# Performance work log

Measured on AMD Instinct MI355X. Metric: run time of the kernel, lower is better.

## Reference

```python
import jax, jax.numpy as jnp
import numpy as np

B_, T_, DIM, HID, OUT, TAG = 128, 256, 512, 1024, 512, 64

def hard_sigmoid(x):
    return jnp.clip(0.2 * x + 0.5, 0.0, 1.0)

def setup_inputs() -> dict:
    key = jax.random.key(0)
    ks = jax.random.split(key, 8)
    s = 0.02  # weight scale for numerical stability under softmax
    return {
        "x": jax.random.normal(ks[0], (B_, T_, DIM), jnp.float32),
        "x0": jnp.zeros((B_, OUT), jnp.float32),
        "s0": jnp.zeros((B_, HID), jnp.float32),
        "W": jax.random.normal(ks[1], (OUT, 3 * HID), jnp.float32) * s,
        "U": jax.random.normal(ks[2], (HID, 3 * HID), jnp.float32) * s,
        "b": jnp.zeros((3 * HID,), jnp.float32),
        "W_x": jax.random.normal(ks[3], (HID, OUT), jnp.float32) * s,
        "b_x": jnp.zeros((OUT,), jnp.float32),
        "V_r": jax.random.normal(ks[4], (DIM, HID), jnp.float32) * s,
        "V_z": jax.random.normal(ks[5], (DIM, HID), jnp.float32) * s,
        "V_s": jax.random.normal(ks[6], (DIM, HID), jnp.float32) * s,
        "W_y": jax.random.normal(ks[7], (OUT, TAG), jnp.float32) * s,
        "b_y": jnp.zeros((TAG,), jnp.float32),
    }

def reference(x, x0, s0, W, U, b, W_x, b_x, V_r, V_z, V_s, W_y, b_y):
    h = HID
    W_r, W_z, W_s = W[:, :h], W[:, h:2*h], W[:, 2*h:]
    U_r, U_z, U_s = U[:, :h], U[:, h:2*h], U[:, 2*h:]
    b_r, b_z, b_s = b[:h], b[h:2*h], b[2*h:]

    def step(carry, inp):
        x_tm1, s_tm1 = carry
        xr = x_tm1 @ W_r + b_r + inp @ V_r
        xz = x_tm1 @ W_z + b_z + inp @ V_z
        r = hard_sigmoid(xr + s_tm1 @ U_r)
        z = hard_sigmoid(xz + s_tm1 @ U_z)
        xs = x_tm1 @ W_s + b_s + inp @ V_s
        s1 = jnp.tanh(xs + (r * s_tm1) @ U_s)
        s_t = (1.0 - z) * s_tm1 + z * s1
        x_t = jax.nn.softmax(s_t @ W_x + b_x, axis=-1)
        t_t = jax.nn.softmax(x_t @ W_y + b_y, axis=-1)
        return (x_t, s_t), t_t

    xs_seq = jnp.swapaxes(x, 0, 1)  # [T, B, dim]
    (_, _), t_seq = jax.lax.scan(step, (x0, s0), xs_seq)
    return jnp.swapaxes(t_seq, 0, 1)  # [B, T, tag]
```

## Files before the change

kernel.cpp:

```cpp
#include <hip/hip_runtime.h>
#include <math.h>

#define B_    128
#define T_    256
#define DIM_  512
#define HID_  1024
#define OUT_  512
#define TAG_  64
#define K3_   3072

typedef float f32x4 __attribute__((ext_vector_type(4)));
typedef short bf16x8 __attribute__((ext_vector_type(8)));

#define MFMA(a,b,c) __builtin_amdgcn_mfma_f32_16x16x32_bf16(a,b,c,0,0,0)

__device__ __forceinline__ unsigned short f2b(float f){
    unsigned int u = __float_as_uint(f);
    u = (u + 0x7fffu + ((u >> 16) & 1u)) >> 16;
    return (unsigned short)u;
}
__device__ __forceinline__ float hardsig(float x){
    return fminf(fmaxf(0.2f*x + 0.5f, 0.f), 1.f);
}
__device__ __forceinline__ bf16x8 ld8(const unsigned short* p){
    return *(const bf16x8*)p;
}
__device__ __forceinline__ bf16x8 ld8f(const float* p){
    float4 a = *(const float4*)p;
    float4 b = *(const float4*)(p + 4);
    bf16x8 r;
    r[0]=(short)f2b(a.x); r[1]=(short)f2b(a.y); r[2]=(short)f2b(a.z); r[3]=(short)f2b(a.w);
    r[4]=(short)f2b(b.x); r[5]=(short)f2b(b.y); r[6]=(short)f2b(b.z); r[7]=(short)f2b(b.w);
    return r;
}

__global__ __launch_bounds__(256) void k_tr(
    unsigned short* __restrict__ dst, const float* __restrict__ src,
    int K, int ld, int col_off)
{
    __shared__ float tile[32][33];
    const int kb = blockIdx.x * 32, nb = blockIdx.y * 32;
    const int tx = threadIdx.x & 31, ty = threadIdx.x >> 5;
    #pragma unroll
    for (int i = 0; i < 4; ++i){
        int kl = ty + i*8;
        tile[kl][tx] = src[(size_t)(kb + kl)*ld + col_off + nb + tx];
    }
    __syncthreads();
    #pragma unroll
    for (int i = 0; i < 4; ++i){
        int nl = ty + i*8;
        dst[(size_t)(nb + nl)*K + kb + tx] = f2b(tile[tx][nl]);
    }
}

__global__ __launch_bounds__(256) void k_cvtx(
    const float4* __restrict__ src, ushort4* __restrict__ dst, int n4)
{
    int i = blockIdx.x * 256 + threadIdx.x;
    if (i < n4){
        float4 v = src[i];
        ushort4 o;
        o.x = f2b(v.x); o.y = f2b(v.y); o.z = f2b(v.z); o.w = f2b(v.w);
        dst[i] = o;
    }
}

__global__ __launch_bounds__(256) void k_init(
    const float* __restrict__ x0, const float* __restrict__ s0,
    unsigned short* __restrict__ xbuf_b, float* __restrict__ sb0,
    unsigned short* __restrict__ s_b)
{
    int i = blockIdx.x * 256 + threadIdx.x;
    if (i < B_*OUT_) xbuf_b[i] = f2b(x0[i]);
    if (i < B_*HID_){ sb0[i] = s0[i]; s_b[i] = f2b(s0[i]); }
}

__global__ __launch_bounds__(256) void k_gemmA(
    const unsigned short* __restrict__ xbuf_b,
    const unsigned short* __restrict__ xb16,
    const float* __restrict__ xf,
    const unsigned short* __restrict__ s_b,
    const float* __restrict__ sp,
    const unsigned short* __restrict__ Wt,
    const unsigned short* __restrict__ Vrt,
    const unsigned short* __restrict__ Vzt,
    const unsigned short* __restrict__ Vst,
    const unsigned short* __restrict__ Urzt,
    const float* __restrict__ bias,
    float* __restrict__ pre,
    unsigned short* __restrict__ rs_b,
    int t, int use_xb)
{
    const int wid  = (blockIdx.x * 256 + threadIdx.x) >> 6;
    const int lane = threadIdx.x & 63;
    const int mt   = wid & 7;
    const int nt   = wid >> 3;
    const int n0   = nt * 32;
    const int nseg = n0 >> 10;
    const int l15  = lane & 15;
    const int kch  = lane >> 4;
    const int arow = mt*16 + l15;
    f32x4 acc0 = {0.f,0.f,0.f,0.f};
    f32x4 acc1 = {0.f,0.f,0.f,0.f};

    {
        const unsigned short* ab = xbuf_b + arow*OUT_ + kch*8;
        const unsigned short* b0 = Wt + (size_t)(n0 + l15)*OUT_ + kch*8;
        const unsigned short* b1 = b0 + 16*OUT_;
        #pragma unroll 4
        for (int kb = 0; kb < OUT_; kb += 32){
            bf16x8 a = ld8(ab + kb);
            acc0 = MFMA(a, ld8(b0 + kb), acc0);
            acc1 = MFMA(a, ld8(b1 + kb), acc1);
        }
    }
    {
        const unsigned short* Vt = (nseg==0) ? Vrt : ((nseg==1) ? Vzt : Vst);
        const int nl = n0 - (nseg << 10);
        const unsigned short* b0 = Vt + (size_t)(nl + l15)*DIM_ + kch*8;
        const unsigned short* b1 = b0 + 16*DIM_;
        if (use_xb){
            const unsigned short* ab = xb16 + ((size_t)arow*T_ + t)*DIM_ + kch*8;
            #pragma unroll 4
            for (int kb = 0; kb < DIM_; kb += 32){
                bf16x8 a = ld8(ab + kb);
                acc0 = MFMA(a, ld8(b0 + kb), acc0);
                acc1 = MFMA(a, ld8(b1 + kb), acc1);
            }
        } else {
            const float* af = xf + ((size_t)arow*T_ + t)*DIM_ + kch*8;
            #pragma unroll 2
            for (int kb = 0; kb < DIM_; kb += 32){
                bf16x8 a = ld8f(af + kb);
                acc0 = MFMA(a, ld8(b0 + kb), acc0);
                acc1 = MFMA(a, ld8(b1 + kb), acc1);
            }
        }
    }
    if (nseg < 2){
        const unsigned short* ab = s_b + arow*HID_ + kch*8;
        const unsigned short* b0 = Urzt + (size_t)(n0 + l15)*HID_ + kch*8;
        const unsigned short* b1 = b0 + 16*HID_;
        #pragma unroll 4
        for (int kb = 0; kb < HID_; kb += 32){
            bf16x8 a = ld8(ab + kb);
            acc0 = MFMA(a, ld8(b0 + kb), acc0);
            acc1 = MFMA(a, ld8(b1 + kb), acc1);
        }
    }
    const int rbase = mt*16 + kch*4;
    #pragma unroll
    for (int half = 0; half < 2; ++half){
        f32x4 acc = half ? acc1 : acc0;
        const int col = n0 + half*16 + l15;
        const float bv = bias[col];
        #pragma unroll
        for (int q = 0; q < 4; ++q){
            const int r = rbase + q;
            const float v = acc[q] + bv;
            if (nseg == 0){
                float rs = hardsig(v) * sp[r*HID_ + col];
                rs_b[r*HID_ + col] = f2b(rs);
            } else {
                pre[(size_t)r*K3_ + col] = v;
            }
        }
    }
}

__global__ __launch_bounds__(256) void k_gemmB(
    const unsigned short* __restrict__ rs_b,
    const unsigned short* __restrict__ Ust,
    const float* __restrict__ pre,
    const float* __restrict__ sp,
    float* __restrict__ snf,
    unsigned short* __restrict__ s_b)
{
    const int wid  = (blockIdx.x * 256 + threadIdx.x) >> 6;
    const int lane = threadIdx.x & 63;
    const int mt = wid & 7;
    const int nt = wid >> 3;
    const int n0 = nt * 32;
    const int l15 = lane & 15;
    const int kch = lane >> 4;
    const int arow = mt*16 + l15;
    f32x4 acc0 = {0.f,0.f,0.f,0.f};
    f32x4 acc1 = {0.f,0.f,0.f,0.f};
    const unsigned short* ab = rs_b + arow*HID_ + kch*8;
    const unsigned short* b0 = Ust + (size_t)(n0 + l15)*HID_ + kch*8;
    const unsigned short* b1 = b0 + 16*HID_;
    #pragma unroll 4
    for (int kb = 0; kb < HID_; kb += 32){
        bf16x8 a = ld8(ab + kb);
        acc0 = MFMA(a, ld8(b0 + kb), acc0);
        acc1 = MFMA(a, ld8(b1 + kb), acc1);
    }
    const int rbase = mt*16 + kch*4;
    #pragma unroll
    for (int half = 0; half < 2; ++half){
        f32x4 acc = half ? acc1 : acc0;
        const int col = n0 + half*16 + l15;
        #pragma unroll
        for (int q = 0; q < 4; ++q){
            const int r = rbase + q;
            float z  = hardsig(pre[(size_t)r*K3_ + HID_ + col]);
            float xs = pre[(size_t)r*K3_ + 2*HID_ + col];
            float so = sp[r*HID_ + col];
            float s1 = tanhf(xs + acc[q]);
            float sn = (1.f - z)*so + z*s1;
            snf[r*HID_ + col] = sn;
            s_b[r*HID_ + col] = f2b(sn);
        }
    }
}

__global__ __launch_bounds__(256) void k_gemmC(
    const unsigned short* __restrict__ s_b,
    const unsigned short* __restrict__ Wxt,
    const float* __restrict__ bx,
    float* __restrict__ logits)
{
    const int wid  = (blockIdx.x * 256 + threadIdx.x) >> 6;
    const int lane = threadIdx.x & 63;
    const int mt = wid & 7;
    const int nt = wid >> 3;
    const int n0 = nt * 32;
    const int l15 = lane & 15;
    const int kch = lane >> 4;
    const int arow = mt*16 + l15;
    f32x4 acc0 = {0.f,0.f,0.f,0.f};
    f32x4 acc1 = {0.f,0.f,0.f,0.f};
    const unsigned short* ab = s_b + arow*HID_ + kch*8;
    const unsigned short* b0 = Wxt + (size_t)(n0 + l15)*HID_ + kch*8;
    const unsigned short* b1 = b0 + 16*HID_;
    #pragma unroll 4
    for (int kb = 0; kb < HID_; kb += 32){
        bf16x8 a = ld8(ab + kb);
        acc0 = MFMA(a, ld8(b0 + kb), acc0);
        acc1 = MFMA(a, ld8(b1 + kb), acc1);
    }
    const int rbase = mt*16 + kch*4;
    #pragma unroll
    for (int half = 0; half < 2; ++half){
        f32x4 acc = half ? acc1 : acc0;
        const int col = n0 + half*16 + l15;
        #pragma unroll
        for (int q = 0; q < 4; ++q){
            logits[(rbase + q)*OUT_ + col] = acc[q] + bx[col];
        }
    }
}

__global__ __launch_bounds__(256) void k_soft(
    const float* __restrict__ logits, const float* __restrict__ Wy,
    const float* __restrict__ by, unsigned short* __restrict__ xbuf_b,
    float* __restrict__ out, int t)
{
    __shared__ float xs[512];
    __shared__ float red[256];
    const int r = blockIdx.x, tid = threadIdx.x;
    float v0 = logits[r*OUT_ + tid];
    float v1 = logits[r*OUT_ + 256 + tid];
    red[tid] = fmaxf(v0, v1);
    __syncthreads();
    for (int s = 128; s > 0; s >>= 1){
        if (tid < s) red[tid] = fmaxf(red[tid], red[tid+s]);
        __syncthreads();
    }
    float mx = red[0];
    __syncthreads();
    float e0 = expf(v0 - mx), e1 = expf(v1 - mx);
    red[tid] = e0 + e1;
    __syncthreads();
    for (int s = 128; s > 0; s >>= 1){
        if (tid < s) red[tid] += red[tid+s];
        __syncthreads();
    }
    float inv = 1.f / red[0];
    __syncthreads();
    float x0v = e0*inv, x1v = e1*inv;
    xs[tid]       = x0v;
    xs[tid + 256] = x1v;
    xbuf_b[r*OUT_ + tid]       = f2b(x0v);
    xbuf_b[r*OUT_ + 256 + tid] = f2b(x1v);
    __syncthreads();
    const int j = tid & 63, part = tid >> 6;
    float p = 0.f;
    const int k0 = part * 128;
    #pragma unroll 4
    for (int k = k0; k < k0 + 128; ++k) p += xs[k] * Wy[k*TAG_ + j];
    red[tid] = p;
    __syncthreads();
    if (tid < 64){
        float tl = red[tid] + red[tid+64] + red[tid+128] + red[tid+192] + by[tid];
        float wm = tl;
        #pragma unroll
        for (int off = 32; off > 0; off >>= 1) wm = fmaxf(wm, __shfl_xor(wm, off));
        float ex = expf(tl - wm);
        float sm = ex;
        #pragma unroll
        for (int off = 32; off > 0; off >>= 1) sm += __shfl_xor(sm, off);
        out[((long)r*T_ + t)*TAG_ + tid] = ex / sm;
    }
}

extern "C" void kernel_launch(void* const* d_in, const int* in_sizes, int n_in,
                              void* d_out, int out_size, void* d_ws, size_t ws_size,
                              hipStream_t stream){
    const float* x   = (const float*)d_in[0];
    const float* x0  = (const float*)d_in[1];
    const float* s0  = (const float*)d_in[2];
    const float* W   = (const float*)d_in[3];
    const float* U   = (const float*)d_in[4];
    const float* b   = (const float*)d_in[5];
    const float* Wx  = (const float*)d_in[6];
    const float* bx  = (const float*)d_in[7];
    const float* Vr  = (const float*)d_in[8];
    const float* Vz  = (const float*)d_in[9];
    const float* Vs  = (const float*)d_in[10];
    const float* Wy  = (const float*)d_in[11];
    const float* by  = (const float*)d_in[12];
    float* out = (float*)d_out;

    char* ws = (char*)d_ws;
    size_t off = 0;
    auto alloc = [&](size_t bytes) -> size_t {
        size_t o = off; off = (off + bytes + 255) & ~(size_t)255; return o;
    };
    unsigned short* Wt     = (unsigned short*)(ws + alloc((size_t)K3_*OUT_*2));
    unsigned short* Urzt   = (unsigned short*)(ws + alloc((size_t)2048*HID_*2));
    unsigned short* Ust    = (unsigned short*)(ws + alloc((size_t)HID_*HID_*2));
    unsigned short* Vrt    = (unsigned short*)(ws + alloc((size_t)HID_*DIM_*2));
    unsigned short* Vzt    = (unsigned short*)(ws + alloc((size_t)HID_*DIM_*2));
    unsigned short* Vst    = (unsigned short*)(ws + alloc((size_t)HID_*DIM_*2));
    unsigned short* Wxt    = (unsigned short*)(ws + alloc((size_t)OUT_*HID_*2));
    unsigned short* xbuf_b = (unsigned short*)(ws + alloc((size_t)B_*OUT_*2));
    unsigned short* s_b    = (unsigned short*)(ws + alloc((size_t)B_*HID_*2));
    unsigned short* rs_b   = (unsigned short*)(ws + alloc((size_t)B_*HID_*2));
    float* sb0    = (float*)(ws + alloc((size_t)B_*HID_*4));
    float* sb1    = (float*)(ws + alloc((size_t)B_*HID_*4));
    float* pre    = (float*)(ws + alloc((size_t)B_*K3_*4));
    float* logits = (float*)(ws + alloc((size_t)B_*OUT_*4));
    size_t base_need = off;
    unsigned short* xb16 = (unsigned short*)(ws + alloc((size_t)B_*T_*DIM_*2));
    const int use_xb = (off <= ws_size) ? 1 : 0;
    (void)base_need;

    k_tr<<<dim3(OUT_/32, K3_/32),  256, 0, stream>>>(Wt,   W,  OUT_, K3_, 0);
    k_tr<<<dim3(HID_/32, 2048/32), 256, 0, stream>>>(Urzt, U,  HID_, K3_, 0);
    k_tr<<<dim3(HID_/32, HID_/32), 256, 0, stream>>>(Ust,  U,  HID_, K3_, 2048);
    k_tr<<<dim3(DIM_/32, HID_/32), 256, 0, stream>>>(Vrt,  Vr, DIM_, HID_, 0);
    k_tr<<<dim3(DIM_/32, HID_/32), 256, 0, stream>>>(Vzt,  Vz, DIM_, HID_, 0);
    k_tr<<<dim3(DIM_/32, HID_/32), 256, 0, stream>>>(Vst,  Vs, DIM_, HID_, 0);
    k_tr<<<dim3(HID_/32, OUT_/32), 256, 0, stream>>>(Wxt,  Wx, HID_, OUT_, 0);
    if (use_xb){
        int n4 = B_*T_*DIM_/4;
        k_cvtx<<<(n4 + 255)/256, 256, 0, stream>>>((const float4*)x, (ushort4*)xb16, n4);
    }
    k_init<<<(B_*HID_ + 255)/256, 256, 0, stream>>>(x0, s0, xbuf_b, sb0, s_b);

    for (int t = 0; t < T_; ++t){
        float* sp = (t & 1) ? sb1 : sb0;
        float* sn = (t & 1) ? sb0 : sb1;
        k_gemmA<<<192, 256, 0, stream>>>(xbuf_b, xb16, x, s_b, sp,
                                         Wt, Vrt, Vzt, Vst, Urzt, b,
                                         pre, rs_b, t, use_xb);
        k_gemmB<<<64, 256, 0, stream>>>(rs_b, Ust, pre, sp, sn, s_b);
        k_gemmC<<<32, 256, 0, stream>>>(s_b, Wxt, bx, logits);
        k_soft <<<128, 256, 0, stream>>>(logits, Wy, by, xbuf_b, out, t);
    }
}
```

Before: 17.24 ms.

## Replace per-timestep kernel launches with one persistent cooperative kernel

Replaces the 1024 small per-step launches (four kernels for each of 256 steps) with a single persistent cooperative kernel of 96 workgroups. The stages are separated by an atomic-counter grid barrier with acquire/release semantics. This removes launch overhead and the inter-kernel gaps on the serial recurrence. In exchange it adds a spin-barrier cost four times per step, and later stages leave many workgroups idle. A launch failure falls back to the old multi-kernel loop.

```diff
diff --git a/kernel.cpp b/kernel.cpp
--- a/kernel.cpp
+++ b/kernel.cpp
@@ -8,6 +8,7 @@
 #define OUT_  512
 #define TAG_  64
 #define K3_   3072
+#define NWG_  96
 
 typedef float f32x4 __attribute__((ext_vector_type(4)));
 typedef short bf16x8 __attribute__((ext_vector_type(8)));
@@ -34,6 +35,16 @@
     return r;
 }
 
+__device__ __forceinline__ void gsync(unsigned* cnt, unsigned target){
+    __syncthreads();
+    if (threadIdx.x == 0){
+        __hip_atomic_fetch_add(cnt, 1u, __ATOMIC_RELEASE, __HIP_MEMORY_SCOPE_AGENT);
+        while (__hip_atomic_load(cnt, __ATOMIC_ACQUIRE, __HIP_MEMORY_SCOPE_AGENT) < target)
+            __builtin_amdgcn_s_sleep(2);
+    }
+    __syncthreads();
+}
+
 __global__ __launch_bounds__(256) void k_tr(
     unsigned short* __restrict__ dst, const float* __restrict__ src,
     int K, int ld, int col_off)
@@ -76,34 +87,234 @@
     if (i < B_*HID_){ sb0[i] = s0[i]; s_b[i] = f2b(s0[i]); }
 }
 
+__global__ __launch_bounds__(512, 1) void k_persist(
+    const unsigned short* __restrict__ xb16, const float* __restrict__ xf, int use_xb,
+    const unsigned short* __restrict__ Wt,  const unsigned short* __restrict__ Vrt,
+    const unsigned short* __restrict__ Vzt, const unsigned short* __restrict__ Vst,
+    const unsigned short* __restrict__ Urzt,const unsigned short* __restrict__ Ust,
+    const unsigned short* __restrict__ Wxt,
+    const float* __restrict__ bias, const float* __restrict__ bx,
+    const float* __restrict__ Wy,   const float* __restrict__ by,
+    unsigned short* __restrict__ xbuf_b, unsigned short* __restrict__ s_b,
+    unsigned short* __restrict__ rs_b,
+    float* __restrict__ sb0, float* __restrict__ sb1,
+    float* __restrict__ pre, float* __restrict__ logits,
+    float* __restrict__ out, unsigned* __restrict__ cnt)
+{
+    const int wg   = blockIdx.x;
+    const int tid  = threadIdx.x;
+    const int lane = tid & 63;
+    const int wv   = tid >> 6;
+    const int l15  = lane & 15;
+    const int kch  = lane >> 4;
+    unsigned target = 0;
+
+    __shared__ float sm_xs[512];
+    __shared__ float sm_red[512];
+
+    for (int t = 0; t < T_; ++t){
+        const float* sp = (t & 1) ? sb1 : sb0;
+        float*       sn = (t & 1) ? sb0 : sb1;
+
+        {
+            const int n0   = wg * 32;
+            const int nseg = n0 >> 10;
+            const int arow = wv*16 + l15;
+            f32x4 acc0 = {0.f,0.f,0.f,0.f};
+            f32x4 acc1 = {0.f,0.f,0.f,0.f};
+            {
+                const unsigned short* ab = xbuf_b + arow*OUT_ + kch*8;
+                const unsigned short* b0 = Wt + (size_t)(n0 + l15)*OUT_ + kch*8;
+                const unsigned short* b1 = b0 + 16*OUT_;
+                #pragma unroll 4
+                for (int kb = 0; kb < OUT_; kb += 32){
+                    bf16x8 a = ld8(ab + kb);
+                    acc0 = MFMA(a, ld8(b0 + kb), acc0);
+                    acc1 = MFMA(a, ld8(b1 + kb), acc1);
+                }
+            }
+            {
+                const unsigned short* Vt = (nseg==0) ? Vrt : ((nseg==1) ? Vzt : Vst);
+                const int nl = n0 - (nseg << 10);
+                const unsigned short* b0 = Vt + (size_t)(nl + l15)*DIM_ + kch*8;
+                const unsigned short* b1 = b0 + 16*DIM_;
+                if (use_xb){
+                    const unsigned short* ab = xb16 + ((size_t)arow*T_ + t)*DIM_ + kch*8;
+                    #pragma unroll 4
+                    for (int kb = 0; kb < DIM_; kb += 32){
+                        bf16x8 a = ld8(ab + kb);
+                        acc0 = MFMA(a, ld8(b0 + kb), acc0);
+                        acc1 = MFMA(a, ld8(b1 + kb), acc1);
+                    }
+                } else {
+                    const float* af = xf + ((size_t)arow*T_ + t)*DIM_ + kch*8;
+                    #pragma unroll 2
+                    for (int kb = 0; kb < DIM_; kb += 32){
+                        bf16x8 a = ld8f(af + kb);
+                        acc0 = MFMA(a, ld8(b0 + kb), acc0);
+                        acc1 = MFMA(a, ld8(b1 + kb), acc1);
+                    }
+                }
+            }
+            if (nseg < 2){
+                const unsigned short* ab = s_b + arow*HID_ + kch*8;
+                const unsigned short* b0 = Urzt + (size_t)(n0 + l15)*HID_ + kch*8;
+                const unsigned short* b1 = b0 + 16*HID_;
+                #pragma unroll 4
+                for (int kb = 0; kb < HID_; kb += 32){
+                    bf16x8 a = ld8(ab + kb);
+                    acc0 = MFMA(a, ld8(b0 + kb), acc0);
+                    acc1 = MFMA(a, ld8(b1 + kb), acc1);
+                }
+            }
+            const int rbase = wv*16 + kch*4;
+            #pragma unroll
+            for (int half = 0; half < 2; ++half){
+                f32x4 acc = half ? acc1 : acc0;
+                const int col = n0 + half*16 + l15;
+                const float bv = bias[col];
+                #pragma unroll
+                for (int q = 0; q < 4; ++q){
+                    const int r = rbase + q;
+                    const float v = acc[q] + bv;
+                    if (nseg == 0){
+                        float rs = hardsig(v) * sp[r*HID_ + col];
+                        rs_b[r*HID_ + col] = f2b(rs);
+                    } else {
+                        pre[(size_t)r*K3_ + col] = v;
+                    }
+                }
+            }
+        }
+        target += NWG_; gsync(cnt, target);
+
+        if (wg < 32){
+            const int n0 = wg * 32;
+            const int arow = wv*16 + l15;
+            f32x4 acc0 = {0.f,0.f,0.f,0.f};
+            f32x4 acc1 = {0.f,0.f,0.f,0.f};
+            const unsigned short* ab = rs_b + arow*HID_ + kch*8;
+            const unsigned short* b0 = Ust + (size_t)(n0 + l15)*HID_ + kch*8;
+            const unsigned short* b1 = b0 + 16*HID_;
+            #pragma unroll 4
+            for (int kb = 0; kb < HID_; kb += 32){
+                bf16x8 a = ld8(ab + kb);
+                acc0 = MFMA(a, ld8(b0 + kb), acc0);
+                acc1 = MFMA(a, ld8(b1 + kb), acc1);
+            }
+            const int rbase = wv*16 + kch*4;
+            #pragma unroll
+            for (int half = 0; half < 2; ++half){
+                f32x4 acc = half ? acc1 : acc0;
+                const int col = n0 + half*16 + l15;
+                #pragma unroll
+                for (int q = 0; q < 4; ++q){
+                    const int r = rbase + q;
+                    float z  = hardsig(pre[(size_t)r*K3_ + HID_ + col]);
+                    float xs = pre[(size_t)r*K3_ + 2*HID_ + col];
+                    float so = sp[r*HID_ + col];
+                    float s1 = tanhf(xs + acc[q]);
+                    float snv = (1.f - z)*so + z*s1;
+                    sn[r*HID_ + col] = snv;
+                    s_b[r*HID_ + col] = f2b(snv);
+                }
+            }
+        }
+        target += NWG_; gsync(cnt, target);
+
+        if (wg < 16){
+            const int n0 = wg * 32;
+            const int arow = wv*16 + l15;
+            f32x4 acc0 = {0.f,0.f,0.f,0.f};
+            f32x4 acc1 = {0.f,0.f,0.f,0.f};
+            const unsigned short* ab = s_b + arow*HID_ + kch*8;
+            const unsigned short* b0 = Wxt + (size_t)(n0 + l15)*HID_ + kch*8;
+            const unsigned short* b1 = b0 + 16*HID_;
+            #pragma unroll 4
+            for (int kb = 0; kb < HID_; kb += 32){
+                bf16x8 a = ld8(ab + kb);
+                acc0 = MFMA(a, ld8(b0 + kb), acc0);
+                acc1 = MFMA(a, ld8(b1 + kb), acc1);
+            }
+            const int rbase = wv*16 + kch*4;
+            #pragma unroll
+            for (int half = 0; half < 2; ++half){
+                f32x4 acc = half ? acc1 : acc0;
+                const int col = n0 + half*16 + l15;
+                #pragma unroll
+                for (int q = 0; q < 4; ++q){
+                    logits[(rbase + q)*OUT_ + col] = acc[q] + bx[col];
+                }
+            }
+        }
+        target += NWG_; gsync(cnt, target);
+
+        for (int r = wg; r < B_; r += NWG_){
+            float v = logits[r*OUT_ + tid];
+            float m = v;
+            #pragma unroll
+            for (int off = 32; off > 0; off >>= 1) m = fmaxf(m, __shfl_xor(m, off));
+            if (lane == 0) sm_red[wv] = m;
+            __syncthreads();
+            float mx = sm_red[0];
+            #pragma unroll
+            for (int q = 1; q < 8; ++q) mx = fmaxf(mx, sm_red[q]);
+            float e = expf(v - mx);
+            float ssum = e;
+            #pragma unroll
+            for (int off = 32; off > 0; off >>= 1) ssum += __shfl_xor(ssum, off);
+            __syncthreads();
+            if (lane == 0) sm_red[wv] = ssum;
+            __syncthreads();
+            float tot = 0.f;
+            #pragma unroll
+            for (int q = 0; q < 8; ++q) tot += sm_red[q];
+            float xv = e / tot;
+            sm_xs[tid] = xv;
+            xbuf_b[r*OUT_ + tid] = f2b(xv);
+            __syncthreads();
+            const int tag = tid & 63, part = tid >> 6;
+            float p = 0.f;
+            const int k0 = part * 64;
+            #pragma unroll 4
+            for (int k = k0; k < k0 + 64; ++k) p += sm_xs[k] * Wy[k*TAG_ + tag];
+            sm_red[tid] = p;
+            __syncthreads();
+            if (tid < 64){
+                float tl = by[tid];
+                #pragma unroll
+                for (int q = 0; q < 8; ++q) tl += sm_red[q*64 + tid];
+                float wm = tl;
+                #pragma unroll
+                for (int off = 32; off > 0; off >>= 1) wm = fmaxf(wm, __shfl_xor(wm, off));
+                float ex = expf(tl - wm);
+                float sm = ex;
+                #pragma unroll
+                for (int off = 32; off > 0; off >>= 1) sm += __shfl_xor(sm, off);
+                out[((long)r*T_ + t)*TAG_ + tid] = ex / sm;
+            }
+            __syncthreads();
+        }
+        target += NWG_; gsync(cnt, target);
+    }
+}
+
 __global__ __launch_bounds__(256) void k_gemmA(
-    const unsigned short* __restrict__ xbuf_b,
-    const unsigned short* __restrict__ xb16,
-    const float* __restrict__ xf,
-    const unsigned short* __restrict__ s_b,
-    const float* __restrict__ sp,
-    const unsigned short* __restrict__ Wt,
-    const unsigned short* __restrict__ Vrt,
-    const unsigned short* __restrict__ Vzt,
-    const unsigned short* __restrict__ Vst,
-    const unsigned short* __restrict__ Urzt,
-    const float* __restrict__ bias,
-    float* __restrict__ pre,
-    unsigned short* __restrict__ rs_b,
-    int t, int use_xb)
+    const unsigned short* __restrict__ xbuf_b, const unsigned short* __restrict__ xb16,
+    const float* __restrict__ xf, const unsigned short* __restrict__ s_b,
+    const float* __restrict__ sp, const unsigned short* __restrict__ Wt,
+    const unsigned short* __restrict__ Vrt, const unsigned short* __restrict__ Vzt,
+    const unsigned short* __restrict__ Vst, const unsigned short* __restrict__ Urzt,
+    const float* __restrict__ bias, float* __restrict__ pre,
+    unsigned short* __restrict__ rs_b, int t, int use_xb)
 {
     const int wid  = (blockIdx.x * 256 + threadIdx.x) >> 6;
     const int lane = threadIdx.x & 63;
-    const int mt   = wid & 7;
-    const int nt   = wid >> 3;
-    const int n0   = nt * 32;
-    const int nseg = n0 >> 10;
-    const int l15  = lane & 15;
-    const int kch  = lane >> 4;
+    const int mt = wid & 7, nt = wid >> 3;
+    const int n0 = nt * 32, nseg = n0 >> 10;
+    const int l15 = lane & 15, kch = lane >> 4;
     const int arow = mt*16 + l15;
-    f32x4 acc0 = {0.f,0.f,0.f,0.f};
-    f32x4 acc1 = {0.f,0.f,0.f,0.f};
-
+    f32x4 acc0 = {0.f,0.f,0.f,0.f}, acc1 = {0.f,0.f,0.f,0.f};
     {
         const unsigned short* ab = xbuf_b + arow*OUT_ + kch*8;
         const unsigned short* b0 = Wt + (size_t)(n0 + l15)*OUT_ + kch*8;
@@ -170,23 +381,17 @@
 }
 
 __global__ __launch_bounds__(256) void k_gemmB(
-    const unsigned short* __restrict__ rs_b,
-    const unsigned short* __restrict__ Ust,
-    const float* __restrict__ pre,
-    const float* __restrict__ sp,
-    float* __restrict__ snf,
-    unsigned short* __restrict__ s_b)
+    const unsigned short* __restrict__ rs_b, const unsigned short* __restrict__ Ust,
+    const float* __restrict__ pre, const float* __restrict__ sp,
+    float* __restrict__ snf, unsigned short* __restrict__ s_b)
 {
     const int wid  = (blockIdx.x * 256 + threadIdx.x) >> 6;
     const int lane = threadIdx.x & 63;
-    const int mt = wid & 7;
-    const int nt = wid >> 3;
+    const int mt = wid & 7, nt = wid >> 3;
     const int n0 = nt * 32;
-    const int l15 = lane & 15;
-    const int kch = lane >> 4;
+    const int l15 = lane & 15, kch = lane >> 4;
     const int arow = mt*16 + l15;
-    f32x4 acc0 = {0.f,0.f,0.f,0.f};
-    f32x4 acc1 = {0.f,0.f,0.f,0.f};
+    f32x4 acc0 = {0.f,0.f,0.f,0.f}, acc1 = {0.f,0.f,0.f,0.f};
     const unsigned short* ab = rs_b + arow*HID_ + kch*8;
     const unsigned short* b0 = Ust + (size_t)(n0 + l15)*HID_ + kch*8;
     const unsigned short* b1 = b0 + 16*HID_;
@@ -208,29 +413,24 @@
             float xs = pre[(size_t)r*K3_ + 2*HID_ + col];
             float so = sp[r*HID_ + col];
             float s1 = tanhf(xs + acc[q]);
-            float sn = (1.f - z)*so + z*s1;
-            snf[r*HID_ + col] = sn;
-            s_b[r*HID_ + col] = f2b(sn);
+            float snv = (1.f - z)*so + z*s1;
+            snf[r*HID_ + col] = snv;
+            s_b[r*HID_ + col] = f2b(snv);
         }
     }
 }
 
 __global__ __launch_bounds__(256) void k_gemmC(
-    const unsigned short* __restrict__ s_b,
-    const unsigned short* __restrict__ Wxt,
-    const float* __restrict__ bx,
-    float* __restrict__ logits)
+    const unsigned short* __restrict__ s_b, const unsigned short* __restrict__ Wxt,
+    const float* __restrict__ bx, float* __restrict__ logits)
 {
     const int wid  = (blockIdx.x * 256 + threadIdx.x) >> 6;
     const int lane = threadIdx.x & 63;
-    const int mt = wid & 7;
-    const int nt = wid >> 3;
+    const int mt = wid & 7, nt = wid >> 3;
     const int n0 = nt * 32;
-    const int l15 = lane & 15;
-    const int kch = lane >> 4;
+    const int l15 = lane & 15, kch = lane >> 4;
     const int arow = mt*16 + l15;
-    f32x4 acc0 = {0.f,0.f,0.f,0.f};
-    f32x4 acc1 = {0.f,0.f,0.f,0.f};
+    f32x4 acc0 = {0.f,0.f,0.f,0.f}, acc1 = {0.f,0.f,0.f,0.f};
     const unsigned short* ab = s_b + arow*HID_ + kch*8;
     const unsigned short* b0 = Wxt + (size_t)(n0 + l15)*HID_ + kch*8;
     const unsigned short* b1 = b0 + 16*HID_;
@@ -280,9 +480,8 @@
     float inv = 1.f / red[0];
     __syncthreads();
     float x0v = e0*inv, x1v = e1*inv;
-    xs[tid]       = x0v;
-    xs[tid + 256] = x1v;
-    xbuf_b[r*OUT_ + tid]       = f2b(x0v);
+    xs[tid] = x0v; xs[tid + 256] = x1v;
+    xbuf_b[r*OUT_ + tid] = f2b(x0v);
     xbuf_b[r*OUT_ + 256 + tid] = f2b(x1v);
     __syncthreads();
     const int j = tid & 63, part = tid >> 6;
@@ -328,25 +527,25 @@
     auto alloc = [&](size_t bytes) -> size_t {
         size_t o = off; off = (off + bytes + 255) & ~(size_t)255; return o;
     };
-    unsigned short* Wt     = (unsigned short*)(ws + alloc((size_t)K3_*OUT_*2));
-    unsigned short* Urzt   = (unsigned short*)(ws + alloc((size_t)2048*HID_*2));
-    unsigned short* Ust    = (unsigned short*)(ws + alloc((size_t)HID_*HID_*2));
-    unsigned short* Vrt    = (unsigned short*)(ws + alloc((size_t)HID_*DIM_*2));
-    unsigned short* Vzt    = (unsigned short*)(ws + alloc((size_t)HID_*DIM_*2));
-    unsigned short* Vst    = (unsigned short*)(ws + alloc((size_t)HID_*DIM_*2));
-    unsigned short* Wxt    = (unsigned short*)(ws + alloc((size_t)OUT_*HID_*2));
-    unsigned short* xbuf_b = (unsigned short*)(ws + alloc((size_t)B_*OUT_*2));
-    unsigned short* s_b    = (unsigned short*)(ws + alloc((size_t)B_*HID_*2));
-    unsigned short* rs_b   = (unsigned short*)(ws + alloc((size_t)B_*HID_*2));
+    unsigned* scnt        = (unsigned*)(ws + alloc(256));
+    unsigned short* Wt    = (unsigned short*)(ws + alloc((size_t)K3_*OUT_*2));
+    unsigned short* Urzt  = (unsigned short*)(ws + alloc((size_t)2048*HID_*2));
+    unsigned short* Ust   = (unsigned short*)(ws + alloc((size_t)HID_*HID_*2));
+    unsigned short* Vrt   = (unsigned short*)(ws + alloc((size_t)HID_*DIM_*2));
+    unsigned short* Vzt   = (unsigned short*)(ws + alloc((size_t)HID_*DIM_*2));
+    unsigned short* Vst   = (unsigned short*)(ws + alloc((size_t)HID_*DIM_*2));
+    unsigned short* Wxt   = (unsigned short*)(ws + alloc((size_t)OUT_*HID_*2));
+    unsigned short* xbuf_b= (unsigned short*)(ws + alloc((size_t)B_*OUT_*2));
+    unsigned short* s_b   = (unsigned short*)(ws + alloc((size_t)B_*HID_*2));
+    unsigned short* rs_b  = (unsigned short*)(ws + alloc((size_t)B_*HID_*2));
     float* sb0    = (float*)(ws + alloc((size_t)B_*HID_*4));
     float* sb1    = (float*)(ws + alloc((size_t)B_*HID_*4));
     float* pre    = (float*)(ws + alloc((size_t)B_*K3_*4));
     float* logits = (float*)(ws + alloc((size_t)B_*OUT_*4));
-    size_t base_need = off;
     unsigned short* xb16 = (unsigned short*)(ws + alloc((size_t)B_*T_*DIM_*2));
-    const int use_xb = (off <= ws_size) ? 1 : 0;
-    (void)base_need;
-
+    int use_xb = (off <= ws_size) ? 1 : 0;
+
+    hipMemsetAsync(scnt, 0, 256, stream);
     k_tr<<<dim3(OUT_/32, K3_/32),  256, 0, stream>>>(Wt,   W,  OUT_, K3_, 0);
     k_tr<<<dim3(HID_/32, 2048/32), 256, 0, stream>>>(Urzt, U,  HID_, K3_, 0);
     k_tr<<<dim3(HID_/32, HID_/32), 256, 0, stream>>>(Ust,  U,  HID_, K3_, 2048);
@@ -360,14 +559,28 @@
     }
     k_init<<<(B_*HID_ + 255)/256, 256, 0, stream>>>(x0, s0, xbuf_b, sb0, s_b);
 
-    for (int t = 0; t < T_; ++t){
-        float* sp = (t & 1) ? sb1 : sb0;
-        float* sn = (t & 1) ? sb0 : sb1;
-        k_gemmA<<<192, 256, 0, stream>>>(xbuf_b, xb16, x, s_b, sp,
-                                         Wt, Vrt, Vzt, Vst, Urzt, b,
-                                         pre, rs_b, t, use_xb);
-        k_gemmB<<<64, 256, 0, stream>>>(rs_b, Ust, pre, sp, sn, s_b);
-        k_gemmC<<<32, 256, 0, stream>>>(s_b, Wxt, bx, logits);
-        k_soft <<<128, 256, 0, stream>>>(logits, Wy, by, xbuf_b, out, t);
-    }
-}
+    const unsigned short* xb16c = xb16;
+    void* kargs[] = {
+        (void*)&xb16c, (void*)&x, (void*)&use_xb,
+        (void*)&Wt, (void*)&Vrt, (void*)&Vzt, (void*)&Vst, (void*)&Urzt, (void*)&Ust,
+        (void*)&Wxt, (void*)&b, (void*)&bx, (void*)&Wy, (void*)&by,
+        (void*)&xbuf_b, (void*)&s_b, (void*)&rs_b,
+        (void*)&sb0, (void*)&sb1, (void*)&pre, (void*)&logits,
+        (void*)&out, (void*)&scnt
+    };
+    hipError_t err = hipLaunchCooperativeKernel((const void*)k_persist,
+                                                dim3(NWG_), dim3(512),
+                                                kargs, 0, stream);
+    if (err != hipSuccess){
+        for (int t = 0; t < T_; ++t){
+            float* sp = (t & 1) ? sb1 : sb0;
+            float* sn = (t & 1) ? sb0 : sb1;
+            k_gemmA<<<192, 256, 0, stream>>>(xbuf_b, xb16, x, s_b, sp,
+                                             Wt, Vrt, Vzt, Vst, Urzt, b,
+                                             pre, rs_b, t, use_xb);
+            k_gemmB<<<64, 256, 0, stream>>>(rs_b, Ust, pre, sp, sn, s_b);
+            k_gemmC<<<32, 256, 0, stream>>>(s_b, Wxt, bx, logits);
+            k_soft <<<128, 256, 0, stream>>>(logits, Wy, by, xbuf_b, out, t);
+        }
+    }
+}
```

Result: slower. 32.12 ms (+86.3%).

## Fuse per-timestep kernels into one persistent cooperative kernel with grid barriers

Applied to the files above, without the earlier changes.

Replaces the four kernel launches per timestep (1024 launches total) with a single persistent cooperative kernel of 96 workgroups that loops over time and uses flag-based grid barriers between the gate GEMM, candidate GEMM, output GEMM and softmax phases. GEMM operands are now staged into swizzled LDS with double-buffered global-to-LDS loads instead of direct global loads per lane. The aim is to remove launch overhead and improve memory access. The cost is fewer active workgroups in later phases (32 and 16 of 96 do GEMM work) and four spin barriers per step.

```diff
diff --git a/kernel.cpp b/kernel.cpp
--- a/kernel.cpp
+++ b/kernel.cpp
@@ -8,11 +8,22 @@
 #define OUT_  512
 #define TAG_  64
 #define K3_   3072
+#define NWG_  96
+#define CK_   128
 
 typedef float f32x4 __attribute__((ext_vector_type(4)));
 typedef short bf16x8 __attribute__((ext_vector_type(8)));
 
 #define MFMA(a,b,c) __builtin_amdgcn_mfma_f32_16x16x32_bf16(a,b,c,0,0,0)
+
+typedef __attribute__((address_space(3))) void       lds_void_t;
+typedef __attribute__((address_space(1))) const void gbl_cvoid_t;
+#define GLOAD_LDS16(g, l) __builtin_amdgcn_global_load_lds((gbl_cvoid_t*)(g), (lds_void_t*)(l), 16, 0, 0)
+
+#define AOFF0 0
+#define AOFF1 32768
+#define BOFF0 65536
+#define BOFF1 73728
 
 __device__ __forceinline__ unsigned short f2b(float f){
     unsigned int u = __float_as_uint(f);
@@ -21,9 +32,6 @@
 }
 __device__ __forceinline__ float hardsig(float x){
     return fminf(fmaxf(0.2f*x + 0.5f, 0.f), 1.f);
-}
-__device__ __forceinline__ bf16x8 ld8(const unsigned short* p){
-    return *(const bf16x8*)p;
 }
 __device__ __forceinline__ bf16x8 ld8f(const float* p){
     float4 a = *(const float4*)p;
@@ -34,6 +42,110 @@
     return r;
 }
 
+__device__ __forceinline__ void gsync(unsigned* flags, unsigned gen, int wg, int tid){
+    __syncthreads();
+    __threadfence();
+    if (tid == 0)
+        __hip_atomic_store(&flags[wg], gen, __ATOMIC_RELAXED, __HIP_MEMORY_SCOPE_AGENT);
+    if (wg == 0){
+        if (tid < NWG_){
+            while (__hip_atomic_load(&flags[tid], __ATOMIC_RELAXED, __HIP_MEMORY_SCOPE_AGENT) != gen)
+                __builtin_amdgcn_s_sleep(2);
+        }
+        __syncthreads();
+        if (tid == 0){
+            __threadfence();
+            __hip_atomic_store(&flags[NWG_], gen, __ATOMIC_RELAXED, __HIP_MEMORY_SCOPE_AGENT);
+        }
+    } else {
+        if (tid == 0){
+            while (__hip_atomic_load(&flags[NWG_], __ATOMIC_RELAXED, __HIP_MEMORY_SCOPE_AGENT) != gen)
+                __builtin_amdgcn_s_sleep(2);
+        }
+    }
+    __syncthreads();
+    __threadfence();
+}
+
+__device__ __forceinline__ void stage_act(
+    char* smem, int off, int wv, int lane,
+    const unsigned short* act, int stride, int k0)
+{
+    const int hi = lane >> 4, l15 = lane & 15;
+    #pragma unroll
+    for (int j = 0; j < 4; ++j){
+        const int i   = wv*4 + j;
+        const int row = i*4 + hi;
+        const int k16 = l15 ^ (row & 7);
+        const unsigned short* src = act + (size_t)row*stride + k0 + k16*8;
+        GLOAD_LDS16(src, smem + off + i*1024);
+    }
+}
+__device__ __forceinline__ void stage_act_f32(
+    char* smem, int off, int wv, int lane,
+    const float* act, int stride, int k0)
+{
+    const int hi = lane >> 4, l15 = lane & 15;
+    #pragma unroll
+    for (int j = 0; j < 4; ++j){
+        const int i   = wv*4 + j;
+        const int row = i*4 + hi;
+        const int k16 = l15 ^ (row & 7);
+        const float* src = act + (size_t)row*stride + k0 + k16*8;
+        bf16x8 v = ld8f(src);
+        *(bf16x8*)(smem + off + i*1024 + lane*16) = v;
+    }
+}
+__device__ __forceinline__ void stage_wgt(
+    char* smem, int off, int wv, int lane,
+    const unsigned short* colbase, int stride, int kloc)
+{
+    const int col = wv*4 + (lane >> 4);
+    const int k16 = (lane & 15) ^ (col & 7);
+    const unsigned short* src = colbase + (size_t)col*stride + kloc + k16*8;
+    GLOAD_LDS16(src, smem + off + wv*1024);
+}
+
+__device__ __forceinline__ void mma_chunk(
+    const char* smem, int aoff, int boff, int wv, int lane,
+    f32x4& acc0, f32x4& acc1)
+{
+    const int l15 = lane & 15, kch = lane >> 4;
+    const int abase = aoff + (wv*16 + l15)*256;
+    const int bbase = boff + l15*256;
+    const int swz = (l15 & 7) << 4;
+    #pragma unroll
+    for (int ks = 0; ks < 4; ++ks){
+        const int kb = (ks*64 + kch*16) ^ swz;
+        bf16x8 a  = *(const bf16x8*)(smem + abase + kb);
+        bf16x8 b0 = *(const bf16x8*)(smem + bbase + kb);
+        bf16x8 b1 = *(const bf16x8*)(smem + bbase + 4096 + kb);
+        acc0 = MFMA(a, b0, acc0);
+        acc1 = MFMA(a, b1, acc1);
+    }
+}
+
+template<class SA, class SB>
+__device__ __forceinline__ void gemm_phase(
+    char* smem, int wv, int lane, int nc, SA&& sA, SB&& sB,
+    f32x4& acc0, f32x4& acc1)
+{
+    sA(AOFF0, 0); sB(BOFF0, 0);
+    asm volatile("s_waitcnt vmcnt(0)" ::: "memory");
+    __syncthreads();
+    int cur = 0;
+    for (int c = 0; c < nc; ++c){
+        if (c + 1 < nc){
+            sA(cur ? AOFF0 : AOFF1, c+1);
+            sB(cur ? BOFF0 : BOFF1, c+1);
+        }
+        mma_chunk(smem, cur ? AOFF1 : AOFF0, cur ? BOFF1 : BOFF0, wv, lane, acc0, acc1);
+        asm volatile("s_waitcnt vmcnt(0)" ::: "memory");
+        __syncthreads();
+        cur ^= 1;
+    }
+}
+
 __global__ __launch_bounds__(256) void k_tr(
     unsigned short* __restrict__ dst, const float* __restrict__ src,
     int K, int ld, int col_off)
@@ -53,7 +165,6 @@
         dst[(size_t)(nb + nl)*K + kb + tx] = f2b(tile[tx][nl]);
     }
 }
-
 __global__ __launch_bounds__(256) void k_cvtx(
     const float4* __restrict__ src, ushort4* __restrict__ dst, int n4)
 {
@@ -65,7 +176,6 @@
         dst[i] = o;
     }
 }
-
 __global__ __launch_bounds__(256) void k_init(
     const float* __restrict__ x0, const float* __restrict__ s0,
     unsigned short* __restrict__ xbuf_b, float* __restrict__ sb0,
@@ -76,232 +186,178 @@
     if (i < B_*HID_){ sb0[i] = s0[i]; s_b[i] = f2b(s0[i]); }
 }
 
-__global__ __launch_bounds__(256) void k_gemmA(
-    const unsigned short* __restrict__ xbuf_b,
-    const unsigned short* __restrict__ xb16,
-    const float* __restrict__ xf,
-    const unsigned short* __restrict__ s_b,
-    const float* __restrict__ sp,
-    const unsigned short* __restrict__ Wt,
-    const unsigned short* __restrict__ Vrt,
-    const unsigned short* __restrict__ Vzt,
-    const unsigned short* __restrict__ Vst,
-    const unsigned short* __restrict__ Urzt,
-    const float* __restrict__ bias,
-    float* __restrict__ pre,
+__global__ __launch_bounds__(512, 1) void k_persist(
+    const unsigned short* __restrict__ xb16, const float* __restrict__ xf, int use_xb,
+    const unsigned short* __restrict__ Wt,  const unsigned short* __restrict__ Vrt,
+    const unsigned short* __restrict__ Vzt, const unsigned short* __restrict__ Vst,
+    const unsigned short* __restrict__ Urzt,const unsigned short* __restrict__ Ust,
+    const unsigned short* __restrict__ Wxt,
+    const float* __restrict__ bias, const float* __restrict__ bx,
+    const float* __restrict__ Wy,   const float* __restrict__ by,
+    unsigned short* __restrict__ xbuf_b, unsigned short* __restrict__ s_b,
     unsigned short* __restrict__ rs_b,
-    int t, int use_xb)
-{
-    const int wid  = (blockIdx.x * 256 + threadIdx.x) >> 6;
-    const int lane = threadIdx.x & 63;
-    const int mt   = wid & 7;
-    const int nt   = wid >> 3;
-    const int n0   = nt * 32;
-    const int nseg = n0 >> 10;
+    float* __restrict__ sb0, float* __restrict__ sb1,
+    float* __restrict__ pre, float* __restrict__ logits,
+    float* __restrict__ out, unsigned* __restrict__ flags)
+{
+    __shared__ __align__(16) char smem[81920];
+    const int wg   = blockIdx.x;
+    const int tid  = threadIdx.x;
+    const int lane = tid & 63;
+    const int wv   = tid >> 6;
     const int l15  = lane & 15;
     const int kch  = lane >> 4;
-    const int arow = mt*16 + l15;
-    f32x4 acc0 = {0.f,0.f,0.f,0.f};
-    f32x4 acc1 = {0.f,0.f,0.f,0.f};
-
-    {
-        const unsigned short* ab = xbuf_b + arow*OUT_ + kch*8;
-        const unsigned short* b0 = Wt + (size_t)(n0 + l15)*OUT_ + kch*8;
-        const unsigned short* b1 = b0 + 16*OUT_;
-        #pragma unroll 4
-        for (int kb = 0; kb < OUT_; kb += 32){
-            bf16x8 a = ld8(ab + kb);
-            acc0 = MFMA(a, ld8(b0 + kb), acc0);
-            acc1 = MFMA(a, ld8(b1 + kb), acc1);
-        }
-    }
-    {
-        const unsigned short* Vt = (nseg==0) ? Vrt : ((nseg==1) ? Vzt : Vst);
-        const int nl = n0 - (nseg << 10);
-        const unsigned short* b0 = Vt + (size_t)(nl + l15)*DIM_ + kch*8;
-        const unsigned short* b1 = b0 + 16*DIM_;
-        if (use_xb){
-            const unsigned short* ab = xb16 + ((size_t)arow*T_ + t)*DIM_ + kch*8;
-            #pragma unroll 4
-            for (int kb = 0; kb < DIM_; kb += 32){
-                bf16x8 a = ld8(ab + kb);
-                acc0 = MFMA(a, ld8(b0 + kb), acc0);
-                acc1 = MFMA(a, ld8(b1 + kb), acc1);
+    unsigned gen = 0;
+
+    const int n0A   = wg * 32;
+    const int nsegA = n0A >> 10;
+    const int ncA   = (nsegA == 2) ? 8 : 16;
+
+    for (int t = 0; t < T_; ++t){
+        const float* sp = (t & 1) ? sb1 : sb0;
+        float*       sn = (t & 1) ? sb0 : sb1;
+
+        {
+            f32x4 acc0 = {0.f,0.f,0.f,0.f}, acc1 = {0.f,0.f,0.f,0.f};
+            auto sA = [&](int off, int c){
+                const int k0 = c*CK_;
+                if (k0 < 512)       stage_act(smem, off, wv, lane, xbuf_b, OUT_, k0);
+                else if (k0 < 1024){
+                    if (use_xb)     stage_act(smem, off, wv, lane, xb16 + (size_t)t*DIM_, T_*DIM_, k0-512);
+                    else            stage_act_f32(smem, off, wv, lane, xf + (size_t)t*DIM_, T_*DIM_, k0-512);
+                } else              stage_act(smem, off, wv, lane, s_b, HID_, k0-1024);
+            };
+            auto sB = [&](int off, int c){
+                const int k0 = c*CK_;
+                const unsigned short* colbase; int stride, kloc;
+                if (k0 < 512){ colbase = Wt + (size_t)n0A*OUT_; stride = OUT_; kloc = k0; }
+                else if (k0 < 1024){
+                    const unsigned short* Vt = (nsegA==0)?Vrt:((nsegA==1)?Vzt:Vst);
+                    colbase = Vt + (size_t)(n0A - (nsegA<<10))*DIM_; stride = DIM_; kloc = k0-512;
+                } else { colbase = Urzt + (size_t)n0A*HID_; stride = HID_; kloc = k0-1024; }
+                stage_wgt(smem, off, wv, lane, colbase, stride, kloc);
+            };
+            gemm_phase(smem, wv, lane, ncA, sA, sB, acc0, acc1);
+
+            const int rbase = wv*16 + kch*4;
+            #pragma unroll
+            for (int half = 0; half < 2; ++half){
+                f32x4 acc = half ? acc1 : acc0;
+                const int col = n0A + half*16 + l15;
+                const float bv = bias[col];
+                #pragma unroll
+                for (int q = 0; q < 4; ++q){
+                    const int r = rbase + q;
+                    const float v = acc[q] + bv;
+                    if (nsegA == 0){
+                        float rs = hardsig(v) * sp[r*HID_ + col];
+                        rs_b[r*HID_ + col] = f2b(rs);
+                    } else {
+                        pre[(size_t)r*K3_ + col] = v;
+                    }
+                }
             }
-        } else {
-            const float* af = xf + ((size_t)arow*T_ + t)*DIM_ + kch*8;
-            #pragma unroll 2
-            for (int kb = 0; kb < DIM_; kb += 32){
-                bf16x8 a = ld8f(af + kb);
-                acc0 = MFMA(a, ld8(b0 + kb), acc0);
-                acc1 = MFMA(a, ld8(b1 + kb), acc1);
+        }
+        gen++; gsync(flags, gen, wg, tid);
+
+        if (wg < 32){
+            const int n0 = wg * 32;
+            f32x4 acc0 = {0.f,0.f,0.f,0.f}, acc1 = {0.f,0.f,0.f,0.f};
+            auto sA = [&](int off, int c){ stage_act(smem, off, wv, lane, rs_b, HID_, c*CK_); };
+            auto sB = [&](int off, int c){ stage_wgt(smem, off, wv, lane, Ust + (size_t)n0*HID_, HID_, c*CK_); };
+            gemm_phase(smem, wv, lane, 8, sA, sB, acc0, acc1);
+
+            const int rbase = wv*16 + kch*4;
+            #pragma unroll
+            for (int half = 0; half < 2; ++half){
+                f32x4 acc = half ? acc1 : acc0;
+                const int col = n0 + half*16 + l15;
+                #pragma unroll
+                for (int q = 0; q < 4; ++q){
+                    const int r = rbase + q;
+                    float z  = hardsig(pre[(size_t)r*K3_ + HID_ + col]);
+                    float xs = pre[(size_t)r*K3_ + 2*HID_ + col];
+                    float so = sp[r*HID_ + col];
+                    float s1 = tanhf(xs + acc[q]);
+                    float snv = (1.f - z)*so + z*s1;
+                    sn[r*HID_ + col] = snv;
+                    s_b[r*HID_ + col] = f2b(snv);
+                }
             }
         }
-    }
-    if (nseg < 2){
-        const unsigned short* ab = s_b + arow*HID_ + kch*8;
-        const unsigned short* b0 = Urzt + (size_t)(n0 + l15)*HID_ + kch*8;
-        const unsigned short* b1 = b0 + 16*HID_;
-        #pragma unroll 4
-        for (int kb = 0; kb < HID_; kb += 32){
-            bf16x8 a = ld8(ab + kb);
-            acc0 = MFMA(a, ld8(b0 + kb), acc0);
-            acc1 = MFMA(a, ld8(b1 + kb), acc1);
-        }
-    }
-    const int rbase = mt*16 + kch*4;
-    #pragma unroll
-    for (int half = 0; half < 2; ++half){
-        f32x4 acc = half ? acc1 : acc0;
-        const int col = n0 + half*16 + l15;
-        const float bv = bias[col];
-        #pragma unroll
-        for (int q = 0; q < 4; ++q){
-            const int r = rbase + q;
-            const float v = acc[q] + bv;
-            if (nseg == 0){
-                float rs = hardsig(v) * sp[r*HID_ + col];
-                rs_b[r*HID_ + col] = f2b(rs);
-            } else {
-                pre[(size_t)r*K3_ + col] = v;
+        gen++; gsync(flags, gen, wg, tid);
+
+        if (wg < 16){
+            const int n0 = wg * 32;
+            f32x4 acc0 = {0.f,0.f,0.f,0.f}, acc1 = {0.f,0.f,0.f,0.f};
+            auto sA = [&](int off, int c){ stage_act(smem, off, wv, lane, s_b, HID_, c*CK_); };
+            auto sB = [&](int off, int c){ stage_wgt(smem, off, wv, lane, Wxt + (size_t)n0*HID_, HID_, c*CK_); };
+            gemm_phase(smem, wv, lane, 8, sA, sB, acc0, acc1);
+
+            const int rbase = wv*16 + kch*4;
+            #pragma unroll
+            for (int half = 0; half < 2; ++half){
+                f32x4 acc = half ? acc1 : acc0;
+                const int col = n0 + half*16 + l15;
+                #pragma unroll
+                for (int q = 0; q < 4; ++q){
+                    logits[(rbase + q)*OUT_ + col] = acc[q] + bx[col];
+                }
             }
         }
-    }
-}
-
-__global__ __launch_bounds__(256) void k_gemmB(
-    const unsigned short* __restrict__ rs_b,
-    const unsigned short* __restrict__ Ust,
-    const float* __restrict__ pre,
-    const float* __restrict__ sp,
-    float* __restrict__ snf,
-    unsigned short* __restrict__ s_b)
-{
-    const int wid  = (blockIdx.x * 256 + threadIdx.x) >> 6;
-    const int lane = threadIdx.x & 63;
-    const int mt = wid & 7;
-    const int nt = wid >> 3;
-    const int n0 = nt * 32;
-    const int l15 = lane & 15;
-    const int kch = lane >> 4;
-    const int arow = mt*16 + l15;
-    f32x4 acc0 = {0.f,0.f,0.f,0.f};
-    f32x4 acc1 = {0.f,0.f,0.f,0.f};
-    const unsigned short* ab = rs_b + arow*HID_ + kch*8;
-    const unsigned short* b0 = Ust + (size_t)(n0 + l15)*HID_ + kch*8;
-    const unsigned short* b1 = b0 + 16*HID_;
-    #pragma unroll 4
-    for (int kb = 0; kb < HID_; kb += 32){
-        bf16x8 a = ld8(ab + kb);
-        acc0 = MFMA(a, ld8(b0 + kb), acc0);
-        acc1 = MFMA(a, ld8(b1 + kb), acc1);
-    }
-    const int rbase = mt*16 + kch*4;
-    #pragma unroll
-    for (int half = 0; half < 2; ++half){
-        f32x4 acc = half ? acc1 : acc0;
-        const int col = n0 + half*16 + l15;
-        #pragma unroll
-        for (int q = 0; q < 4; ++q){
-            const int r = rbase + q;
-            float z  = hardsig(pre[(size_t)r*K3_ + HID_ + col]);
-            float xs = pre[(size_t)r*K3_ + 2*HID_ + col];
-            float so = sp[r*HID_ + col];
-            float s1 = tanhf(xs + acc[q]);
-            float sn = (1.f - z)*so + z*s1;
-            snf[r*HID_ + col] = sn;
-            s_b[r*HID_ + col] = f2b(sn);
-        }
-    }
-}
-
-__global__ __launch_bounds__(256) void k_gemmC(
-    const unsigned short* __restrict__ s_b,
-    const unsigned short* __restrict__ Wxt,
-    const float* __restrict__ bx,
-    float* __restrict__ logits)
-{
-    const int wid  = (blockIdx.x * 256 + threadIdx.x) >> 6;
-    const int lane = threadIdx.x & 63;
-    const int mt = wid & 7;
-    const int nt = wid >> 3;
-    const int n0 = nt * 32;
-    const int l15 = lane & 15;
-    const int kch = lane >> 4;
-    const int arow = mt*16 + l15;
-    f32x4 acc0 = {0.f,0.f,0.f,0.f};
-    f32x4 acc1 = {0.f,0.f,0.f,0.f};
-    const unsigned short* ab = s_b + arow*HID_ + kch*8;
-    const unsigned short* b0 = Wxt + (size_t)(n0 + l15)*HID_ + kch*8;
-    const unsigned short* b1 = b0 + 16*HID_;
-    #pragma unroll 4
-    for (int kb = 0; kb < HID_; kb += 32){
-        bf16x8 a = ld8(ab + kb);
-        acc0 = MFMA(a, ld8(b0 + kb), acc0);
-        acc1 = MFMA(a, ld8(b1 + kb), acc1);
-    }
-    const int rbase = mt*16 + kch*4;
-    #pragma unroll
-    for (int half = 0; half < 2; ++half){
-        f32x4 acc = half ? acc1 : acc0;
-        const int col = n0 + half*16 + l15;
-        #pragma unroll
-        for (int q = 0; q < 4; ++q){
-            logits[(rbase + q)*OUT_ + col] = acc[q] + bx[col];
-        }
-    }
-}
-
-__global__ __launch_bounds__(256) void k_soft(
-    const float* __restrict__ logits, const float* __restrict__ Wy,
-    const float* __restrict__ by, unsigned short* __restrict__ xbuf_b,
-    float* __restrict__ out, int t)
-{
-    __shared__ float xs[512];
-    __shared__ float red[256];
-    const int r = blockIdx.x, tid = threadIdx.x;
-    float v0 = logits[r*OUT_ + tid];
-    float v1 = logits[r*OUT_ + 256 + tid];
-    red[tid] = fmaxf(v0, v1);
-    __syncthreads();
-    for (int s = 128; s > 0; s >>= 1){
-        if (tid < s) red[tid] = fmaxf(red[tid], red[tid+s]);
-        __syncthreads();
-    }
-    float mx = red[0];
-    __syncthreads();
-    float e0 = expf(v0 - mx), e1 = expf(v1 - mx);
-    red[tid] = e0 + e1;
-    __syncthreads();
-    for (int s = 128; s > 0; s >>= 1){
-        if (tid < s) red[tid] += red[tid+s];
-        __syncthreads();
-    }
-    float inv = 1.f / red[0];
-    __syncthreads();
-    float x0v = e0*inv, x1v = e1*inv;
-    xs[tid]       = x0v;
-    xs[tid + 256] = x1v;
-    xbuf_b[r*OUT_ + tid]       = f2b(x0v);
-    xbuf_b[r*OUT_ + 256 + tid] = f2b(x1v);
-    __syncthreads();
-    const int j = tid & 63, part = tid >> 6;
-    float p = 0.f;
-    const int k0 = part * 128;
-    #pragma unroll 4
-    for (int k = k0; k < k0 + 128; ++k) p += xs[k] * Wy[k*TAG_ + j];
-    red[tid] = p;
-    __syncthreads();
-    if (tid < 64){
-        float tl = red[tid] + red[tid+64] + red[tid+128] + red[tid+192] + by[tid];
-        float wm = tl;
-        #pragma unroll
-        for (int off = 32; off > 0; off >>= 1) wm = fmaxf(wm, __shfl_xor(wm, off));
-        float ex = expf(tl - wm);
-        float sm = ex;
-        #pragma unroll
-        for (int off = 32; off > 0; off >>= 1) sm += __shfl_xor(sm, off);
-        out[((long)r*T_ + t)*TAG_ + tid] = ex / sm;
+        gen++; gsync(flags, gen, wg, tid);
+
+        {
+            float* sm_xs  = (float*)smem;
+            float* sm_red = (float*)(smem + 2048);
+            for (int r = wg; r < B_; r += NWG_){
+                float v = logits[r*OUT_ + tid];
+                float m = v;
+                #pragma unroll
+                for (int off = 32; off > 0; off >>= 1) m = fmaxf(m, __shfl_xor(m, off));
+                if (lane == 0) sm_red[wv] = m;
+                __syncthreads();
+                float mx = sm_red[0];
+                #pragma unroll
+                for (int q = 1; q < 8; ++q) mx = fmaxf(mx, sm_red[q]);
+                float e = expf(v - mx);
+                float ssum = e;
+                #pragma unroll
+                for (int off = 32; off > 0; off >>= 1) ssum += __shfl_xor(ssum, off);
+                __syncthreads();
+                if (lane == 0) sm_red[wv] = ssum;
+                __syncthreads();
+                float tot = 0.f;
+                #pragma unroll
+                for (int q = 0; q < 8; ++q) tot += sm_red[q];
+                float xv = e / tot;
+                sm_xs[tid] = xv;
+                xbuf_b[r*OUT_ + tid] = f2b(xv);
+                __syncthreads();
+                const int tag = tid & 63, part = tid >> 6;
+                float p = 0.f;
+                const int k0 = part * 64;
+                #pragma unroll 4
+                for (int k = k0; k < k0 + 64; ++k) p += sm_xs[k] * Wy[k*TAG_ + tag];
+                sm_red[tid] = p;
+                __syncthreads();
+                if (tid < 64){
+                    float tl = by[tid];
+                    #pragma unroll
+                    for (int q = 0; q < 8; ++q) tl += sm_red[q*64 + tid];
+                    float wm = tl;
+                    #pragma unroll
+                    for (int off = 32; off > 0; off >>= 1) wm = fmaxf(wm, __shfl_xor(wm, off));
+                    float ex = expf(tl - wm);
+                    float sm = ex;
+                    #pragma unroll
+                    for (int off = 32; off > 0; off >>= 1) sm += __shfl_xor(sm, off);
+                    out[((long)r*T_ + t)*TAG_ + tid] = ex / sm;
+                }
+                __syncthreads();
+            }
+        }
+        gen++; gsync(flags, gen, wg, tid);
     }
 }
 
@@ -328,25 +384,25 @@
     auto alloc = [&](size_t bytes) -> size_t {
         size_t o = off; off = (off + bytes + 255) & ~(size_t)255; return o;
     };
-    unsigned short* Wt     = (unsigned short*)(ws + alloc((size_t)K3_*OUT_*2));
-    unsigned short* Urzt   = (unsigned short*)(ws + alloc((size_t)2048*HID_*2));
-    unsigned short* Ust    = (unsigned short*)(ws + alloc((size_t)HID_*HID_*2));
-    unsigned short* Vrt    = (unsigned short*)(ws + alloc((size_t)HID_*DIM_*2));
-    unsigned short* Vzt    = (unsigned short*)(ws + alloc((size_t)HID_*DIM_*2));
-    unsigned short* Vst    = (unsigned short*)(ws + alloc((size_t)HID_*DIM_*2));
-    unsigned short* Wxt    = (unsigned short*)(ws + alloc((size_t)OUT_*HID_*2));
-    unsigned short* xbuf_b = (unsigned short*)(ws + alloc((size_t)B_*OUT_*2));
-    unsigned short* s_b    = (unsigned short*)(ws + alloc((size_t)B_*HID_*2));
-    unsigned short* rs_b   = (unsigned short*)(ws + alloc((size_t)B_*HID_*2));
+    unsigned* flags       = (unsigned*)(ws + alloc(512));
+    unsigned short* Wt    = (unsigned short*)(ws + alloc((size_t)K3_*OUT_*2));
+    unsigned short* Urzt  = (unsigned short*)(ws + alloc((size_t)2048*HID_*2));
+    unsigned short* Ust   = (unsigned short*)(ws + alloc((size_t)HID_*HID_*2));
+    unsigned short* Vrt   = (unsigned short*)(ws + alloc((size_t)HID_*DIM_*2));
+    unsigned short* Vzt   = (unsigned short*)(ws + alloc((size_t)HID_*DIM_*2));
+    unsigned short* Vst   = (unsigned short*)(ws + alloc((size_t)HID_*DIM_*2));
+    unsigned short* Wxt   = (unsigned short*)(ws + alloc((size_t)OUT_*HID_*2));
+    unsigned short* xbuf_b= (unsigned short*)(ws + alloc((size_t)B_*OUT_*2));
+    unsigned short* s_b   = (unsigned short*)(ws + alloc((size_t)B_*HID_*2));
+    unsigned short* rs_b  = (unsigned short*)(ws + alloc((size_t)B_*HID_*2));
     float* sb0    = (float*)(ws + alloc((size_t)B_*HID_*4));
     float* sb1    = (float*)(ws + alloc((size_t)B_*HID_*4));
     float* pre    = (float*)(ws + alloc((size_t)B_*K3_*4));
     float* logits = (float*)(ws + alloc((size_t)B_*OUT_*4));
-    size_t base_need = off;
     unsigned short* xb16 = (unsigned short*)(ws + alloc((size_t)B_*T_*DIM_*2));
-    const int use_xb = (off <= ws_size) ? 1 : 0;
-    (void)base_need;
-
+    int use_xb = (off <= ws_size) ? 1 : 0;
+
+    hipMemsetAsync(flags, 0, 512, stream);
     k_tr<<<dim3(OUT_/32, K3_/32),  256, 0, stream>>>(Wt,   W,  OUT_, K3_, 0);
     k_tr<<<dim3(HID_/32, 2048/32), 256, 0, stream>>>(Urzt, U,  HID_, K3_, 0);
     k_tr<<<dim3(HID_/32, HID_/32), 256, 0, stream>>>(Ust,  U,  HID_, K3_, 2048);
@@ -360,14 +416,21 @@
     }
     k_init<<<(B_*HID_ + 255)/256, 256, 0, stream>>>(x0, s0, xbuf_b, sb0, s_b);
 
-    for (int t = 0; t < T_; ++t){
-        float* sp = (t & 1) ? sb1 : sb0;
-        float* sn = (t & 1) ? sb0 : sb1;
-        k_gemmA<<<192, 256, 0, stream>>>(xbuf_b, xb16, x, s_b, sp,
-                                         Wt, Vrt, Vzt, Vst, Urzt, b,
-                                         pre, rs_b, t, use_xb);
-        k_gemmB<<<64, 256, 0, stream>>>(rs_b, Ust, pre, sp, sn, s_b);
-        k_gemmC<<<32, 256, 0, stream>>>(s_b, Wxt, bx, logits);
-        k_soft <<<128, 256, 0, stream>>>(logits, Wy, by, xbuf_b, out, t);
-    }
-}
+    const unsigned short* xb16c = xb16;
+    void* kargs[] = {
+        (void*)&xb16c, (void*)&x, (void*)&use_xb,
+        (void*)&Wt, (void*)&Vrt, (void*)&Vzt, (void*)&Vst, (void*)&Urzt, (void*)&Ust,
+        (void*)&Wxt, (void*)&b, (void*)&bx, (void*)&Wy, (void*)&by,
+        (void*)&xbuf_b, (void*)&s_b, (void*)&rs_b,
+        (void*)&sb0, (void*)&sb1, (void*)&pre, (void*)&logits,
+        (void*)&out, (void*)&flags
+    };
+    hipError_t err = hipLaunchCooperativeKernel((const void*)k_persist,
+                                                dim3(NWG_), dim3(512),
+                                                kargs, 0, stream);
+    if (err != hipSuccess){
+        k_persist<<<NWG_, 512, 0, stream>>>(
+            xb16c, x, use_xb, Wt, Vrt, Vzt, Vst, Urzt, Ust, Wxt,
+            b, bx, Wy, by, xbuf_b, s_b, rs_b, sb0, sb1, pre, logits, out, flags);
+    }
+}
```

Result: slower. 35.08 ms (+103.5%).
